# Performance work log

Measured on AMD Instinct MI355X. Metric: run time of the kernel, lower is better.

The kernel has to match this reference:

```python
import jax, jax.numpy as jnp
import numpy as np

B, T, H = 32, 2048, 512


def setup_inputs() -> dict:
    key = jax.random.key(0)
    ks = jax.random.split(key, 6)
    s = 1.0 / np.sqrt(T)  # keep tanh/softmax in a sane range (glorot-ish)
    return {
        "x": jax.random.normal(ks[0], (B, T, H), dtype=jnp.float32),
        "t": jax.random.normal(ks[1], (B, T, H), dtype=jnp.float32),
        "kernel_x": jax.random.normal(ks[2], (T, T), dtype=jnp.float32) * s,
        "kernel_t": jax.random.normal(ks[3], (T, T), dtype=jnp.float32) * s,
        "kernel_a": jax.random.normal(ks[4], (T, T), dtype=jnp.float32) * s,
        "bias_x": jnp.zeros((T,), dtype=jnp.float32),
        "bias_t": jnp.zeros((T,), dtype=jnp.float32),
        "lambd": jax.random.uniform(ks[5], (H, 1), dtype=jnp.float32),
    }


def reference(x, t, kernel_x, kernel_t, kernel_a, bias_x, bias_t, lambd):
    # Permute (2,1): [B, T, H] -> [B, H, T]
    xp = jnp.swapaxes(x, 1, 2)
    tp = jnp.swapaxes(t, 1, 2)
    # gamma/beta: [B, H, T] @ [T, T] + bias, then tanh
    gamma = jnp.tanh(jnp.einsum('bht,ts->bhs', xp, kernel_x) + bias_x)
    beta = jnp.tanh(jnp.einsum('bht,ts->bhs', tp, kernel_t) + bias_t)
    # Convex combination with learned lambd [H, 1] broadcasting over T
    delta = lambd * gamma + (1.0 - lambd) * beta
    # Attention weights: softmax over last (timestamp) axis
    alpha = jax.nn.softmax(jnp.einsum('bht,ts->bhs', delta, kernel_a), axis=-1)
    # Permute back: [B, H, T] -> [B, T, H]
    return jnp.swapaxes(alpha, 1, 2)
```

## Files before the change

kernel.cpp:

```cpp
#include <hip/hip_runtime.h>

constexpr int Bc = 32, Tc = 2048, Hc = 512;

typedef _Float16 f16;
typedef _Float16 f16x8 __attribute__((ext_vector_type(8)));
typedef float f32x4 __attribute__((ext_vector_type(4)));

__device__ __forceinline__ void gload_lds16(const void* g, void* l) {
  __builtin_amdgcn_global_load_lds(
      (const __attribute__((address_space(1))) void*)g,
      (__attribute__((address_space(3))) void*)l, 16, 0, 0);
}

__device__ __forceinline__ float fast_exp(float x) {
  return __builtin_amdgcn_exp2f(x * 1.4426950408889634f);
}
__device__ __forceinline__ float fast_tanh(float x) {
  const float z = __builtin_amdgcn_exp2f(x * 2.8853900817779268f);
  return (z - 1.0f) * __builtin_amdgcn_rcpf(z + 1.0f);
}

__global__ __launch_bounds__(256) void cvt_bth(const float* __restrict__ xin,
                                               const float* __restrict__ tin,
                                               f16* __restrict__ xo,
                                               f16* __restrict__ to) {
  __shared__ f16 tile[64][65];
  const int tid = threadIdx.x;
  const int t0 = blockIdx.x * 64, h0 = blockIdx.y * 64;
  int z = blockIdx.z;
  const float* src;
  f16* dst;
  if (z < Bc) { src = xin; dst = xo; } else { src = tin; dst = to; z -= Bc; }
  src += (size_t)z * Tc * Hc;
  dst += (size_t)z * Hc * Tc;
  const int c4 = tid & 15, r0 = tid >> 4;
#pragma unroll
  for (int rr = 0; rr < 64; rr += 16) {
    const float4 v = *(const float4*)(src + (size_t)(t0 + rr + r0) * Hc + h0 + c4 * 4);
    tile[rr + r0][c4 * 4 + 0] = (f16)v.x;
    tile[rr + r0][c4 * 4 + 1] = (f16)v.y;
    tile[rr + r0][c4 * 4 + 2] = (f16)v.z;
    tile[rr + r0][c4 * 4 + 3] = (f16)v.w;
  }
  __syncthreads();
  const int tc = tid & 7, hr = tid >> 3;
#pragma unroll
  for (int hp = 0; hp < 64; hp += 32) {
    const int h = hp + hr;
    f16x8 o;
#pragma unroll
    for (int j = 0; j < 8; ++j) o[j] = tile[tc * 8 + j][h];
    *(f16x8*)(dst + (size_t)(h0 + h) * Tc + t0 + tc * 8) = o;
  }
}

__global__ __launch_bounds__(256) void cvt_tt(const float* __restrict__ kx,
                                              const float* __restrict__ kt,
                                              const float* __restrict__ ka,
                                              f16* __restrict__ ox,
                                              f16* __restrict__ ot,
                                              f16* __restrict__ oa) {
  __shared__ f16 tile[64][65];
  const int tid = threadIdx.x;
  const int t0 = blockIdx.x * 64, s0 = blockIdx.y * 64;
  const float* src = blockIdx.z == 0 ? kx : (blockIdx.z == 1 ? kt : ka);
  f16* dst = blockIdx.z == 0 ? ox : (blockIdx.z == 1 ? ot : oa);
  const int c4 = tid & 15, r0 = tid >> 4;
#pragma unroll
  for (int rr = 0; rr < 64; rr += 16) {
    const float4 v = *(const float4*)(src + (size_t)(t0 + rr + r0) * Tc + s0 + c4 * 4);
    tile[rr + r0][c4 * 4 + 0] = (f16)v.x;
    tile[rr + r0][c4 * 4 + 1] = (f16)v.y;
    tile[rr + r0][c4 * 4 + 2] = (f16)v.z;
    tile[rr + r0][c4 * 4 + 3] = (f16)v.w;
  }
  __syncthreads();
  const int tc = tid & 7, sr = tid >> 3;
#pragma unroll
  for (int sp = 0; sp < 64; sp += 32) {
    const int s = sp + sr;
    f16x8 o;
#pragma unroll
    for (int j = 0; j < 8; ++j) o[j] = tile[tc * 8 + j][s];
    *(f16x8*)(dst + (size_t)(s0 + s) * Tc + t0 + tc * 8) = o;
  }
}

template <int MODE>
__global__ __launch_bounds__(512, 2) void gemm_k(const f16* __restrict__ A,
                                                 const f16* __restrict__ Bm,
                                                 void* __restrict__ Cout,
                                                 const f16* __restrict__ Gprev,
                                                 const float* __restrict__ bias,
                                                 const float* __restrict__ lambd,
                                                 float* __restrict__ psums) {
  extern __shared__ char smem[];
  constexpr int BK = 64, NT = Tc / BK;
  const int tid = threadIdx.x;
  const int lane = tid & 63, w = tid >> 6;
  const int wr = w >> 2, wc = w & 3;
  const int l15 = lane & 15, kg = lane >> 4;

  int id = (int)blockIdx.x;
  id = (id & 7) * ((int)gridDim.x >> 3) + (id >> 3);
  int b, m0, n0;
  if constexpr (MODE == 2) {
    b = id >> 4; m0 = ((id >> 1) & 7) * 256; n0 = (id & 1) * 256;
  } else {
    b = 0; m0 = (id >> 3) * 256; n0 = (id & 7) * 256;
  }

  const size_t K = Tc;
  const size_t HT = (size_t)Hc * Tc;
  const f16* Ag = A + (size_t)m0 * K;
  const f16* Bg = Bm + (MODE == 2 ? (size_t)b * HT : (size_t)0) + (size_t)n0 * K;

  const int srow = w * 16 + (lane >> 2);
  const int cswz = ((lane & 3) ^ ((lane >> 3) & 3)) * 8;
  const f16* gAs = Ag + (size_t)srow * K + cswz;
  const f16* gBs = Bg + (size_t)srow * K + cswz;
  char* stW = smem + w * 1024;

#define STG(op, h, ktile, d, g)                                                        \
  gload_lds16(((op) ? gBs : gAs) + (size_t)(h) * 128 * Tc + (size_t)(ktile) * BK + (g) * 32, \
              stW + (d) * 65536 + (op) * 32768 + (h) * 16384 + (g) * 8192)
#define STGH(op, h, ktile, d) do { STG(op, h, ktile, d, 0); STG(op, h, ktile, d, 1); } while (0)

  const int chunk16 = (kg ^ ((l15 >> 1) & 3)) * 16;
  const char* pA0 = smem + wr * 16384 + l15 * 64 + chunk16;
  const char* pA1 = pA0 + 65536;
  const char* pB0 = smem + 32768 + (wc >> 1) * 16384 + ((wc & 1) * 64 + l15) * 64 + chunk16;
  const char* pB1 = pB0 + 65536;

  f32x4 acc[8][4];
#pragma unroll
  for (int i = 0; i < 8; ++i)
#pragma unroll
    for (int j = 0; j < 4; ++j) acc[i][j] = {0.f, 0.f, 0.f, 0.f};

  f16x8 b00, b01, b10, b11, b20, b21, b30, b31;
  f16x8 alo0, alo1, ahi0, ahi1;

#define RD_B(P) do {                                     \
    b00 = *(const f16x8*)((P));                          \
    b01 = *(const f16x8*)((P) + 8192);                   \
    b10 = *(const f16x8*)((P) + 1024);                   \
    b11 = *(const f16x8*)((P) + 8192 + 1024);            \
    b20 = *(const f16x8*)((P) + 2048);                   \
    b21 = *(const f16x8*)((P) + 8192 + 2048);            \
    b30 = *(const f16x8*)((P) + 3072);                   \
    b31 = *(const f16x8*)((P) + 8192 + 3072); } while (0)

#define RD_A(P, MI2) do {                                \
    alo0 = *(const f16x8*)((P) + (MI2) * 1024);          \
    alo1 = *(const f16x8*)((P) + 8192 + (MI2) * 1024);   \
    ahi0 = *(const f16x8*)((P) + (MI2 + 1) * 1024);      \
    ahi1 = *(const f16x8*)((P) + 8192 + (MI2 + 1) * 1024); } while (0)

#define MFMA_(a, bq, d) d = __builtin_amdgcn_mfma_f32_16x16x32_f16(a, bq, d, 0, 0, 0)
#define MM8(MI2) do {                                    \
    MFMA_(alo0, b00, acc[MI2][0]); MFMA_(alo0, b10, acc[MI2][1]);         \
    MFMA_(alo0, b20, acc[MI2][2]); MFMA_(alo0, b30, acc[MI2][3]);         \
    MFMA_(ahi0, b00, acc[MI2 + 1][0]); MFMA_(ahi0, b10, acc[MI2 + 1][1]); \
    MFMA_(ahi0, b20, acc[MI2 + 1][2]); MFMA_(ahi0, b30, acc[MI2 + 1][3]); \
    MFMA_(alo1, b01, acc[MI2][0]); MFMA_(alo1, b11, acc[MI2][1]);         \
    MFMA_(alo1, b21, acc[MI2][2]); MFMA_(alo1, b31, acc[MI2][3]);         \
    MFMA_(ahi1, b01, acc[MI2 + 1][0]); MFMA_(ahi1, b11, acc[MI2 + 1][1]); \
    MFMA_(ahi1, b21, acc[MI2 + 1][2]); MFMA_(ahi1, b31, acc[MI2 + 1][3]); } while (0)

#define BAR __builtin_amdgcn_s_barrier()
#define SP1 __builtin_amdgcn_s_setprio(1)
#define SP0 __builtin_amdgcn_s_setprio(0)

  STGH(1, 0, 0, 0); STGH(1, 1, 0, 0); STGH(0, 0, 0, 0); STGH(0, 1, 0, 0);
  STGH(1, 0, 1, 1); STGH(1, 1, 1, 1);
  asm volatile("s_waitcnt vmcnt(4)");
  BAR;
  __builtin_amdgcn_sched_barrier(0);

  for (int it = 0; it < NT / 2; ++it) {
    const int u = 2 * it, vT = u + 1;
    const bool full = (it < NT / 2 - 1);
    RD_B(pB0); RD_A(pA0, 0);
    STGH(0, 0, vT, 1);
    BAR; SP1; MM8(0); SP0; BAR;
    RD_A(pA0, 2);
    STGH(0, 1, vT, 1);
    if (full) STGH(1, 0, u + 2, 0);
    BAR; SP1; MM8(2); SP0; BAR;
    RD_A(pA0, 4);
    if (full) STGH(1, 1, u + 2, 0);
    BAR; SP1; MM8(4); SP0; BAR;
    RD_A(pA0, 6);
    BAR; SP1; MM8(6); SP0;
    if (full) { asm volatile("s_waitcnt vmcnt(4)"); }
    else      { asm volatile("s_waitcnt vmcnt(0)"); }
    BAR;
    __builtin_amdgcn_sched_barrier(0);
    RD_B(pB1); RD_A(pA1, 0);
    if (full) STGH(0, 0, u + 2, 0);
    BAR; SP1; MM8(0); SP0; BAR;
    RD_A(pA1, 2);
    if (full) { STGH(0, 1, u + 2, 0); STGH(1, 0, vT + 2, 1); }
    BAR; SP1; MM8(2); SP0; BAR;
    RD_A(pA1, 4);
    if (full) STGH(1, 1, vT + 2, 1);
    BAR; SP1; MM8(4); SP0; BAR;
    RD_A(pA1, 6);
    BAR; SP1; MM8(6); SP0;
    if (full) { asm volatile("s_waitcnt vmcnt(4)"); }
    else      { asm volatile("s_waitcnt vmcnt(0)"); }
    BAR;
    __builtin_amdgcn_sched_barrier(0);
  }

  float psum[4] = {0.f, 0.f, 0.f, 0.f};
#pragma unroll
  for (int i = 0; i < 8; ++i) {
#pragma unroll
    for (int r = 0; r < 4; ++r) {
      const int gr = m0 + wr * 128 + i * 16 + kg * 4 + r;
#pragma unroll
      for (int j = 0; j < 4; ++j) {
        const int gc = n0 + wc * 64 + j * 16 + l15;
        const float v = acc[i][j][r];
        if constexpr (MODE == 0) {
          f16* C = (f16*)Cout;
          C[(size_t)gr * Tc + gc] = (f16)fast_tanh(v + bias[gc]);
        } else if constexpr (MODE == 1) {
          f16* C = (f16*)Cout;
          const size_t idx = (size_t)gr * Tc + gc;
          const float g = (float)Gprev[idx];
          const float lam = lambd[gr & 511];
          C[idx] = (f16)(lam * g + (1.f - lam) * fast_tanh(v + bias[gc]));
        } else {
          f16* Es = (f16*)Cout;
          const float e = fast_exp(v);
          Es[((size_t)b * Tc + gr) * Hc + gc] = (f16)e;
          psum[j] += e;
        }
      }
    }
  }
  if constexpr (MODE == 2) {
    float* ps = (float*)smem;
    __syncthreads();
#pragma unroll
    for (int j = 0; j < 4; ++j)
      ps[(wr * 4 + kg) * 256 + (wc * 64 + j * 16 + l15)] = psum[j];
    __syncthreads();
    if (tid < 256) {
      float s = 0.f;
#pragma unroll
      for (int p = 0; p < 8; ++p) s += ps[p * 256 + tid];
      psums[((size_t)b * 8 + (m0 >> 8)) * Hc + n0 + tid] = s;
    }
  }
}

__global__ __launch_bounds__(1024) void norm_k(const f16* __restrict__ Es,
                                               const float* __restrict__ psums,
                                               float* __restrict__ out) {
  __shared__ float inv[512];
  const int tid = threadIdx.x;
  const int b = blockIdx.x >> 4, sseg = blockIdx.x & 15;
  if (tid < 512) {
    float s = 0.f;
    const float* P = psums + (size_t)b * 8 * Hc + tid;
#pragma unroll
    for (int p = 0; p < 8; ++p) s += P[p * Hc];
    inv[tid] = 1.f / s;
  }
  __syncthreads();
  const int hg = (tid & 63) * 8;
  const int so = tid >> 6;
  float iv[8];
#pragma unroll
  for (int j = 0; j < 8; ++j) iv[j] = inv[hg + j];
  const size_t base = ((size_t)b * Tc + sseg * 128) * Hc;
  for (int r = so; r < 128; r += 16) {
    const size_t idx = base + (size_t)r * Hc + hg;
    const f16x8 e = *(const f16x8*)(Es + idx);
    float4 o0, o1;
    o0.x = (float)e[0] * iv[0]; o0.y = (float)e[1] * iv[1];
    o0.z = (float)e[2] * iv[2]; o0.w = (float)e[3] * iv[3];
    o1.x = (float)e[4] * iv[4]; o1.y = (float)e[5] * iv[5];
    o1.z = (float)e[6] * iv[6]; o1.w = (float)e[7] * iv[7];
    *(float4*)(out + idx) = o0;
    *(float4*)(out + idx + 4) = o1;
  }
}

extern "C" void kernel_launch(void* const* d_in, const int* in_sizes, int n_in,
                              void* d_out, int out_size, void* d_ws, size_t ws_size,
                              hipStream_t stream) {
  const float* x  = (const float*)d_in[0];
  const float* tt = (const float*)d_in[1];
  const float* kx = (const float*)d_in[2];
  const float* kt = (const float*)d_in[3];
  const float* ka = (const float*)d_in[4];
  const float* bx = (const float*)d_in[5];
  const float* bt = (const float*)d_in[6];
  const float* lm = (const float*)d_in[7];
  float* out = (float*)d_out;

  const size_t NBHT = (size_t)Bc * Hc * Tc;

  f16* XhT = (f16*)d_out;
  f16* ThT = XhT + NBHT;

  f16* Gt  = (f16*)d_ws;
  f16* Dt  = Gt + NBHT;
  f16* KxT = Dt + NBHT;
  f16* KtT = KxT + (size_t)Tc * Tc;
  f16* KaT = KtT + (size_t)Tc * Tc;
  float* Ps = (float*)KxT;
  f16* Es = Gt;

  constexpr int LDS_BYTES = 131072;
  (void)hipFuncSetAttribute(reinterpret_cast<const void*>(gemm_k<0>),
                            hipFuncAttributeMaxDynamicSharedMemorySize, LDS_BYTES);
  (void)hipFuncSetAttribute(reinterpret_cast<const void*>(gemm_k<1>),
                            hipFuncAttributeMaxDynamicSharedMemorySize, LDS_BYTES);
  (void)hipFuncSetAttribute(reinterpret_cast<const void*>(gemm_k<2>),
                            hipFuncAttributeMaxDynamicSharedMemorySize, LDS_BYTES);

  cvt_bth<<<dim3(Tc / 64, Hc / 64, Bc * 2), 256, 0, stream>>>(x, tt, XhT, ThT);
  cvt_tt<<<dim3(Tc / 64, Tc / 64, 3), 256, 0, stream>>>(kx, kt, ka, KxT, KtT, KaT);
  gemm_k<0><<<512, 512, LDS_BYTES, stream>>>(XhT, KxT, Gt, nullptr, bx, nullptr, nullptr);
  gemm_k<1><<<512, 512, LDS_BYTES, stream>>>(ThT, KtT, Dt, Gt, bt, lm, nullptr);
  gemm_k<2><<<512, 512, LDS_BYTES, stream>>>(KaT, Dt, Es, nullptr, nullptr, nullptr, Ps);
  norm_k<<<dim3(Bc * 16), 1024, 0, stream>>>(Es, Ps, out);
}
```

Before: 517.4 us.

## Load B fragments directly to registers and triple-buffer A in LDS

Restructures the GEMM main loop. B operand fragments are now loaded straight from global memory into registers, with a one-tile lookahead. Only the A tile is staged through LDS, in a three-deep ring buffer with BK reduced to 32. This cuts LDS from 128KB to 48KB and removes many barriers and LDS reads of B, aiming to raise occupancy and overlap. The cost is more global traffic, since each wave reloads B from L2, and a finer-grained pipeline whose vmcnt accounting must stay exactly right.

```diff
diff --git a/kernel.cpp b/kernel.cpp
--- a/kernel.cpp
+++ b/kernel.cpp
@@ -95,7 +95,8 @@
                                                  const float* __restrict__ lambd,
                                                  float* __restrict__ psums) {
   extern __shared__ char smem[];
-  constexpr int BK = 64, NT = Tc / BK;
+  constexpr int BK = 32, NT = Tc / BK;
+  constexpr int ABUF = 16384;
   const int tid = threadIdx.x;
   const int lane = tid & 63, w = tid >> 6;
   const int wr = w >> 2, wc = w & 3;
@@ -115,22 +116,15 @@
   const f16* Ag = A + (size_t)m0 * K;
   const f16* Bg = Bm + (MODE == 2 ? (size_t)b * HT : (size_t)0) + (size_t)n0 * K;
 
-  const int srow = w * 16 + (lane >> 2);
+  const int r4 = lane >> 2;
   const int cswz = ((lane & 3) ^ ((lane >> 3) & 3)) * 8;
-  const f16* gAs = Ag + (size_t)srow * K + cswz;
-  const f16* gBs = Bg + (size_t)srow * K + cswz;
-  char* stW = smem + w * 1024;
-
-#define STG(op, h, ktile, d, g)                                                        \
-  gload_lds16(((op) ? gBs : gAs) + (size_t)(h) * 128 * Tc + (size_t)(ktile) * BK + (g) * 32, \
-              stW + (d) * 65536 + (op) * 32768 + (h) * 16384 + (g) * 8192)
-#define STGH(op, h, ktile, d) do { STG(op, h, ktile, d, 0); STG(op, h, ktile, d, 1); } while (0)
+  const f16* gAs = Ag + (size_t)(w * 32 + r4) * K + cswz;
+  const int ldsW = w * 2048;
 
   const int chunk16 = (kg ^ ((l15 >> 1) & 3)) * 16;
-  const char* pA0 = smem + wr * 16384 + l15 * 64 + chunk16;
-  const char* pA1 = pA0 + 65536;
-  const char* pB0 = smem + 32768 + (wc >> 1) * 16384 + ((wc & 1) * 64 + l15) * 64 + chunk16;
-  const char* pB1 = pB0 + 65536;
+  const int aoff = (wr * 128 + l15) * 64 + chunk16;
+
+  const f16* Bl = Bg + (size_t)(wc * 64 + l15) * K + kg * 8;
 
   f32x4 acc[8][4];
 #pragma unroll
@@ -138,80 +132,66 @@
 #pragma unroll
     for (int j = 0; j < 4; ++j) acc[i][j] = {0.f, 0.f, 0.f, 0.f};
 
-  f16x8 b00, b01, b10, b11, b20, b21, b30, b31;
-  f16x8 alo0, alo1, ahi0, ahi1;
-
-#define RD_B(P) do {                                     \
-    b00 = *(const f16x8*)((P));                          \
-    b01 = *(const f16x8*)((P) + 8192);                   \
-    b10 = *(const f16x8*)((P) + 1024);                   \
-    b11 = *(const f16x8*)((P) + 8192 + 1024);            \
-    b20 = *(const f16x8*)((P) + 2048);                   \
-    b21 = *(const f16x8*)((P) + 8192 + 2048);            \
-    b30 = *(const f16x8*)((P) + 3072);                   \
-    b31 = *(const f16x8*)((P) + 8192 + 3072); } while (0)
-
-#define RD_A(P, MI2) do {                                \
-    alo0 = *(const f16x8*)((P) + (MI2) * 1024);          \
-    alo1 = *(const f16x8*)((P) + 8192 + (MI2) * 1024);   \
-    ahi0 = *(const f16x8*)((P) + (MI2 + 1) * 1024);      \
-    ahi1 = *(const f16x8*)((P) + 8192 + (MI2 + 1) * 1024); } while (0)
+  f16x8 bcE[4], bcO[4], af[8];
+
+#define LOADB(DST, T) do {                                                   \
+    _Pragma("unroll")                                                        \
+    for (int j = 0; j < 4; ++j)                                              \
+      DST[j] = *(const f16x8*)(Bl + (size_t)(j * 16) * K + (size_t)(T) * 32);} while (0)
+
+#define STGA(T) do {                                                         \
+    char* dA = smem + ((T) % 3) * ABUF + ldsW;                               \
+    gload_lds16(gAs + (size_t)(T) * BK, dA);                                 \
+    gload_lds16(gAs + (size_t)16 * K + (size_t)(T) * BK, dA + 1024); } while (0)
 
 #define MFMA_(a, bq, d) d = __builtin_amdgcn_mfma_f32_16x16x32_f16(a, bq, d, 0, 0, 0)
-#define MM8(MI2) do {                                    \
-    MFMA_(alo0, b00, acc[MI2][0]); MFMA_(alo0, b10, acc[MI2][1]);         \
-    MFMA_(alo0, b20, acc[MI2][2]); MFMA_(alo0, b30, acc[MI2][3]);         \
-    MFMA_(ahi0, b00, acc[MI2 + 1][0]); MFMA_(ahi0, b10, acc[MI2 + 1][1]); \
-    MFMA_(ahi0, b20, acc[MI2 + 1][2]); MFMA_(ahi0, b30, acc[MI2 + 1][3]); \
-    MFMA_(alo1, b01, acc[MI2][0]); MFMA_(alo1, b11, acc[MI2][1]);         \
-    MFMA_(alo1, b21, acc[MI2][2]); MFMA_(alo1, b31, acc[MI2][3]);         \
-    MFMA_(ahi1, b01, acc[MI2 + 1][0]); MFMA_(ahi1, b11, acc[MI2 + 1][1]); \
-    MFMA_(ahi1, b21, acc[MI2 + 1][2]); MFMA_(ahi1, b31, acc[MI2 + 1][3]); } while (0)
-
+#define SB __builtin_amdgcn_sched_barrier(0)
 #define BAR __builtin_amdgcn_s_barrier()
 #define SP1 __builtin_amdgcn_s_setprio(1)
 #define SP0 __builtin_amdgcn_s_setprio(0)
 
-  STGH(1, 0, 0, 0); STGH(1, 1, 0, 0); STGH(0, 0, 0, 0); STGH(0, 1, 0, 0);
-  STGH(1, 0, 1, 1); STGH(1, 1, 1, 1);
-  asm volatile("s_waitcnt vmcnt(4)");
+  LOADB(bcE, 0);
+  SB;
+  STGA(0);
+  STGA(1);
+  SB;
+  asm volatile("s_waitcnt vmcnt(2)");
   BAR;
-  __builtin_amdgcn_sched_barrier(0);
-
-  for (int it = 0; it < NT / 2; ++it) {
-    const int u = 2 * it, vT = u + 1;
-    const bool full = (it < NT / 2 - 1);
-    RD_B(pB0); RD_A(pA0, 0);
-    STGH(0, 0, vT, 1);
-    BAR; SP1; MM8(0); SP0; BAR;
-    RD_A(pA0, 2);
-    STGH(0, 1, vT, 1);
-    if (full) STGH(1, 0, u + 2, 0);
-    BAR; SP1; MM8(2); SP0; BAR;
-    RD_A(pA0, 4);
-    if (full) STGH(1, 1, u + 2, 0);
-    BAR; SP1; MM8(4); SP0; BAR;
-    RD_A(pA0, 6);
-    BAR; SP1; MM8(6); SP0;
-    if (full) { asm volatile("s_waitcnt vmcnt(4)"); }
-    else      { asm volatile("s_waitcnt vmcnt(0)"); }
-    BAR;
-    __builtin_amdgcn_sched_barrier(0);
-    RD_B(pB1); RD_A(pA1, 0);
-    if (full) STGH(0, 0, u + 2, 0);
-    BAR; SP1; MM8(0); SP0; BAR;
-    RD_A(pA1, 2);
-    if (full) { STGH(0, 1, u + 2, 0); STGH(1, 0, vT + 2, 1); }
-    BAR; SP1; MM8(2); SP0; BAR;
-    RD_A(pA1, 4);
-    if (full) STGH(1, 1, vT + 2, 1);
-    BAR; SP1; MM8(4); SP0; BAR;
-    RD_A(pA1, 6);
-    BAR; SP1; MM8(6); SP0;
-    if (full) { asm volatile("s_waitcnt vmcnt(4)"); }
-    else      { asm volatile("s_waitcnt vmcnt(0)"); }
-    BAR;
-    __builtin_amdgcn_sched_barrier(0);
+  SB;
+
+#define TILE(T, BCC, BCN) do {                                               \
+    const char* bufc = smem + ((T) % 3) * ABUF;                              \
+    _Pragma("unroll")                                                        \
+    for (int i = 0; i < 8; ++i) af[i] = *(const f16x8*)(bufc + aoff + i * 1024); \
+    if ((T) + 1 < NT) LOADB(BCN, (T) + 1);                                   \
+    SB;                                                                      \
+    if ((T) + 2 < NT) STGA((T) + 2);                                         \
+    SB;                                                                      \
+    if ((T) < NT - 2)       { asm volatile("s_waitcnt vmcnt(8)"); }          \
+    else if ((T) == NT - 2) { asm volatile("s_waitcnt vmcnt(6)"); }          \
+    else                    { asm volatile("s_waitcnt vmcnt(0)"); }          \
+    SP1;                                                                     \
+    _Pragma("unroll")                                                        \
+    for (int i = 0; i < 4; ++i)                                              \
+      _Pragma("unroll")                                                      \
+      for (int j = 0; j < 4; ++j) MFMA_(af[i], BCC[j], acc[i][j]);           \
+    SP0;                                                                     \
+    if ((T) < NT - 2)       { asm volatile("s_waitcnt vmcnt(6)"); }          \
+    else if ((T) == NT - 2) { asm volatile("s_waitcnt vmcnt(4)"); }          \
+    asm volatile("s_waitcnt lgkmcnt(0)");                                    \
+    BAR;                                                                     \
+    SB;                                                                      \
+    SP1;                                                                     \
+    _Pragma("unroll")                                                        \
+    for (int i = 0; i < 4; ++i)                                              \
+      _Pragma("unroll")                                                      \
+      for (int j = 0; j < 4; ++j) MFMA_(af[4 + i], BCC[j], acc[4 + i][j]);   \
+    SP0;                                                                     \
+  } while (0)
+
+  for (int t = 0; t < NT; t += 2) {
+    TILE(t, bcE, bcO);
+    TILE(t + 1, bcO, bcE);
   }
 
   float psum[4] = {0.f, 0.f, 0.f, 0.f};
@@ -317,7 +297,7 @@
   float* Ps = (float*)KxT;
   f16* Es = Gt;
 
-  constexpr int LDS_BYTES = 131072;
+  constexpr int LDS_BYTES = 3 * 16384;
   (void)hipFuncSetAttribute(reinterpret_cast<const void*>(gemm_k<0>),
                             hipFuncAttributeMaxDynamicSharedMemorySize, LDS_BYTES);
   (void)hipFuncSetAttribute(reinterpret_cast<const void*>(gemm_k<1>),
```

Result: slower. 779.4 us (+50.6%).
